# Kernel optimization log

Measured on AMD Instinct MI355X. Metric: run time of the kernel, lower is better.

The kernel has to match this reference:

```python
import jax, jax.numpy as jnp
import numpy as np

B, C, H, W = 8, 256, 128, 128
K = 3  # conv kernel size, padding=1 -> SAME


def conv3x3(x, w, b):
    # x: [B,C,H,W], w: [O,I,K,K], b: [O]
    y = jax.lax.conv_general_dilated(
        x, w, window_strides=(1, 1), padding='SAME',
        dimension_numbers=('NCHW', 'OIHW', 'NCHW'))
    return y + b[None, :, None, None]


def setup_inputs() -> dict:
    key = jax.random.key(0)
    ks = jax.random.split(key, 7)
    fan_in = C * K * K
    s = 1.0 / np.sqrt(fan_in)
    x = jax.random.normal(ks[0], (B, C, H, W), dtype=jnp.float32)
    Wq = jax.random.uniform(ks[1], (C, C, K, K), jnp.float32, -s, s)
    bq = jax.random.uniform(ks[2], (C,), jnp.float32, -s, s)
    Wk = jax.random.uniform(ks[3], (C, C, K, K), jnp.float32, -s, s)
    bk = jax.random.uniform(ks[4], (C,), jnp.float32, -s, s)
    Wv = jax.random.uniform(ks[5], (C, C, K, K), jnp.float32, -s, s)
    bv = jax.random.uniform(ks[6], (C,), jnp.float32, -s, s)
    return {'x': x, 'Wq': Wq, 'bq': bq, 'Wk': Wk, 'bk': bk, 'Wv': Wv, 'bv': bv}


def reference(x, Wq, bq, Wk, bk, Wv, bv):
    b_, c_, h_, w_ = x.shape
    residual = x
    q = jax.nn.relu(conv3x3(x, Wq, bq))  # [B,C,H,W]
    k = jax.nn.relu(conv3x3(x, Wk, bk))  # [B,C,H,W]
    v = conv3x3(x, Wv, bv)               # [B,C,H,W]
    # per-(batch,channel) spatial matmul: [H,W] @ [H,W] -> [H,W] (requires H==W)
    attn = jnp.einsum('bcij,bcjk->bcik', q, k)
    # softmax over the flattened H*W positions jointly per (b,c)
    attn = jax.nn.softmax(attn.reshape(b_, c_, h_ * w_), axis=-1).reshape(b_, c_, h_, w_)
    y = jnp.einsum('bcij,bcjk->bcik', attn, v)
    return y + residual
```

## Files before the change

kernel.cpp:

```cpp
#include <hip/hip_runtime.h>

#define BB 8
#define CC 256
#define HH 128
#define WW 128
#define HW (HH*WW)

typedef float f32x4 __attribute__((ext_vector_type(4)));
typedef float f32x16 __attribute__((ext_vector_type(16)));
typedef short s16x8 __attribute__((ext_vector_type(8)));

__device__ inline unsigned short f2bf(float f) {
  union { float f; unsigned int u; } un;
  un.f = f;
  unsigned int u = un.u;
  return (unsigned short)((u + 0x7fffu + ((u >> 16) & 1u)) >> 16);
}

__device__ __forceinline__ void gload_lds16(const void* g, void* l) {
  __builtin_amdgcn_global_load_lds(
      (const __attribute__((address_space(1))) unsigned int*)g,
      (__attribute__((address_space(3))) unsigned int*)l, 16, 0, 0);
}

__global__ __launch_bounds__(256) void k_prepass(const float* __restrict__ x,
                                                 unsigned short* __restrict__ xbf) {
  __shared__ float tile[64][68];
  int bh = blockIdx.x;
  int b = bh >> 7, h = bh & 127;
  int w0 = blockIdx.y * 64;
  int c0 = blockIdx.z * 64;
  int t = threadIdx.x;
  {
    int c = t >> 2, wq = (t & 3) << 4;
    const float4* src = reinterpret_cast<const float4*>(
        x + (((size_t)(b * CC + c0 + c) * HH + h) * WW + w0 + wq));
    float4 v0 = src[0], v1 = src[1], v2 = src[2], v3 = src[3];
    *reinterpret_cast<float4*>(&tile[c][wq + 0])  = v0;
    *reinterpret_cast<float4*>(&tile[c][wq + 4])  = v1;
    *reinterpret_cast<float4*>(&tile[c][wq + 8])  = v2;
    *reinterpret_cast<float4*>(&tile[c][wq + 12]) = v3;
  }
  __syncthreads();
  {
    int w = t >> 2, cg = (t & 3) << 4;
    unsigned short tmp[16];
#pragma unroll
    for (int i = 0; i < 16; ++i) tmp[i] = f2bf(tile[cg + i][w]);
    unsigned short* dst = xbf + ((size_t)(b * HH + h) * WW + w0 + w) * CC + c0 + cg;
    *reinterpret_cast<int4*>(dst)     = *reinterpret_cast<int4*>(tmp);
    *reinterpret_cast<int4*>(dst + 8) = *reinterpret_cast<int4*>(tmp + 8);
  }
}

__global__ __launch_bounds__(256) void k_repack(const float* __restrict__ Wq,
                                                const float* __restrict__ Wk,
                                                const float* __restrict__ Wv,
                                                unsigned short* __restrict__ Wp,
                                                unsigned short* __restrict__ zp) {
  if (blockIdx.x == 0 && threadIdx.x < 64) {
    int4 z = {0, 0, 0, 0};
    reinterpret_cast<int4*>(zp)[threadIdx.x] = z;
  }
  int idx = blockIdx.x * 256 + threadIdx.x;
  if (idx >= 8 * 9 * 768 * 32) return;
  int ci = idx & 31;
  int tmp = idx >> 5;
  int focs = tmp % 768;
  int tmp2 = tmp / 768;
  int tap = tmp2 % 9;
  int chunk = tmp2 / 9;
  int cv = focs >> 8, oc = focs & 255;
  int cin = chunk * 32 + ci;
  const float* Wsrc = (cv == 0) ? Wq : ((cv == 1) ? Wk : Wv);
  Wp[idx] = f2bf(Wsrc[(size_t)(oc * 256 + cin) * 9 + tap]);
}

__global__ __launch_bounds__(256, 2) void k_conv(const unsigned short* __restrict__ xbf,
                                                 const unsigned short* __restrict__ Wp,
                                                 const unsigned short* __restrict__ zp,
                                                 const float* __restrict__ bq,
                                                 const float* __restrict__ bk,
                                                 const float* __restrict__ bv,
                                                 unsigned short* __restrict__ qkv) {
  __shared__ unsigned short xs[2][4][132][32];
  __shared__ float bias_s[128];
  int bid = blockIdx.x;
  int v_ = (bid & 7) * 384 + (bid >> 3);
  int mtile = v_ % 6;
  int bhp = v_ / 6;
  int b = bhp >> 6;
  int h0 = (bhp & 63) * 2;
  int t = threadIdx.x;
  int lane = t & 63, wave = t >> 6;
  int wm = wave >> 1, wq = wave & 1;
  int l31 = lane & 31, lg1 = lane >> 5;

  if (t < 128) {
    int focs = mtile * 128 + t;
    int cv = focs >> 8, oc = focs & 255;
    const float* bp = (cv == 0) ? bq : ((cv == 1) ? bk : bv);
    bias_s[t] = bp[oc];
  }
  {
    int cell = t >> 4;
    int bf_ = cell >> 3, r_ = (cell >> 1) & 3;
    int wc_ = (cell & 1) ? 129 : 0;
    *reinterpret_cast<int*>(reinterpret_cast<char*>(&xs[bf_][r_][wc_][0]) + (t & 15) * 4) = 0;
  }

  int l2 = lane >> 2, l4 = lane & 3;
  int osw = l4 ^ (((l2 + 1) >> 1) & 3);
  int rsta = wave;
  int hin = h0 + rsta - 1;
  bool inb = ((unsigned)hin < 128u);
  const unsigned short* srow =
      xbf + ((size_t)(b * HH + (inb ? hin : 0)) * WW + l2) * CC + osw * 8;
  const unsigned short* zsrc = zp + lane * 8;

  auto STAGE = [&](int bufn, int chunk) {
    char* d0 = reinterpret_cast<char*>(&xs[bufn][rsta][1][0]);
    if (inb) {
      const unsigned short* s0 = srow + chunk * 32;
#pragma unroll
      for (int j = 0; j < 8; ++j)
        gload_lds16(s0 + j * (16 * CC), d0 + j * 1024);
    } else {
#pragma unroll
      for (int j = 0; j < 8; ++j)
        gload_lds16(zsrc, d0 + j * 1024);
    }
  };

  f32x16 acc[2][2][2] = {};
  STAGE(0, 0);
  __syncthreads();
  int buf = 0;
  for (int chunk = 0; chunk < 8; ++chunk) {
    if (chunk < 7) STAGE(buf ^ 1, chunk + 1);
    const unsigned short (*xsb)[132][32] = xs[buf];
    const unsigned short* ap0 = Wp + (size_t)chunk * (9 * 768 * 32)
        + (size_t)(mtile * 128 + wm * 64 + l31) * 32 + lg1 * 8;
#pragma unroll
    for (int ss = 0; ss < 3; ++ss) {
#pragma unroll
      for (int kk = 0; kk < 2; ++kk) {
        s16x8 Bf[4][2];
#pragma unroll
        for (int rin = 0; rin < 4; ++rin)
#pragma unroll
        for (int nt = 0; nt < 2; ++nt) {
          int wc = wq * 64 + nt * 32 + l31 + ss;
          int pslot = (kk * 2 + lg1) ^ ((wc >> 1) & 3);
          Bf[rin][nt] = *reinterpret_cast<const s16x8*>(
              reinterpret_cast<const char*>(&xsb[rin][0][0]) + wc * 64 + pslot * 16);
        }
        s16x8 Af[3][2];
#pragma unroll
        for (int rr = 0; rr < 3; ++rr)
#pragma unroll
        for (int mt = 0; mt < 2; ++mt)
          Af[rr][mt] = *reinterpret_cast<const s16x8*>(
              ap0 + (rr * 3 + ss) * (768 * 32) + mt * 1024 + kk * 16);
#pragma unroll
        for (int rr = 0; rr < 3; ++rr)
#pragma unroll
        for (int row = 0; row < 2; ++row)
#pragma unroll
        for (int mt = 0; mt < 2; ++mt)
#pragma unroll
        for (int nt = 0; nt < 2; ++nt)
          acc[mt][row][nt] = __builtin_amdgcn_mfma_f32_32x32x16_bf16(
              Af[rr][mt], Bf[row + rr][nt], acc[mt][row][nt], 0, 0, 0);
      }
    }
    if (chunk < 7) __syncthreads();
    buf ^= 1;
  }

#pragma unroll
  for (int mt = 0; mt < 2; ++mt) {
#pragma unroll
    for (int row = 0; row < 2; ++row) {
#pragma unroll
      for (int nt = 0; nt < 2; ++nt) {
        int wcol = wq * 64 + nt * 32 + l31;
        int h = h0 + row;
#pragma unroll
        for (int reg = 0; reg < 16; ++reg) {
          int rloc = (reg & 3) + 8 * (reg >> 2) + 4 * lg1;
          int floc = wm * 64 + mt * 32 + rloc;
          float vv = acc[mt][row][nt][reg] + bias_s[floc];
          int focs = mtile * 128 + floc;
          if (focs < 512) vv = fmaxf(vv, 0.0f);
          int cv = focs >> 8, oc = focs & 255;
          qkv[(size_t)(cv * 2048 + b * 256 + oc) * HW + h * WW + wcol] = f2bf(vv);
        }
      }
    }
  }
}

#define PADA 136
__global__ __launch_bounds__(256) void k_attn(const unsigned short* __restrict__ qkv,
                                              const float* __restrict__ x,
                                              float* __restrict__ out) {
  __shared__ unsigned short al[128][PADA];
  __shared__ unsigned short kt[128][PADA];
  __shared__ unsigned short vt[128][PADA];
  __shared__ float red[8];
  int bc = blockIdx.x;
  const unsigned short* qp = qkv + (size_t)bc * HW;
  const unsigned short* kp = qkv + (size_t)(2048 + bc) * HW;
  const unsigned short* vp = qkv + (size_t)(4096 + bc) * HW;
  int t = threadIdx.x;
  for (int g = t; g < HW; g += 256) {
    int row = g >> 7, col = g & 127;
    kt[col][row] = kp[g];
    vt[col][row] = vp[g];
  }
  __syncthreads();
  int lane = t & 63, wave = t >> 6;
  int wm = wave >> 1, wn = wave & 1;
  int l15 = lane & 15, lg = lane >> 4;
  f32x4 acc[4][4] = {};
#pragma unroll
  for (int kk = 0; kk < 4; ++kk) {
    s16x8 af[4], bfr[4];
#pragma unroll
    for (int m = 0; m < 4; ++m)
      af[m] = *reinterpret_cast<const s16x8*>(qp + (size_t)(wm * 64 + m * 16 + l15) * WW + kk * 32 + lg * 8);
#pragma unroll
    for (int n = 0; n < 4; ++n)
      bfr[n] = *reinterpret_cast<const s16x8*>(&kt[wn * 64 + n * 16 + l15][kk * 32 + lg * 8]);
#pragma unroll
    for (int m = 0; m < 4; ++m)
#pragma unroll
      for (int n = 0; n < 4; ++n)
        acc[m][n] = __builtin_amdgcn_mfma_f32_16x16x32_bf16(af[m], bfr[n], acc[m][n], 0, 0, 0);
  }
  float lm = -3.0e38f;
#pragma unroll
  for (int m = 0; m < 4; ++m)
#pragma unroll
    for (int n = 0; n < 4; ++n)
#pragma unroll
      for (int rg = 0; rg < 4; ++rg)
        lm = fmaxf(lm, acc[m][n][rg]);
  for (int off = 32; off > 0; off >>= 1) lm = fmaxf(lm, __shfl_xor(lm, off));
  if (lane == 0) red[wave] = lm;
  __syncthreads();
  float M = fmaxf(fmaxf(red[0], red[1]), fmaxf(red[2], red[3]));
  float ls = 0.0f;
#pragma unroll
  for (int m = 0; m < 4; ++m)
#pragma unroll
    for (int n = 0; n < 4; ++n)
#pragma unroll
      for (int rg = 0; rg < 4; ++rg)
        ls += __expf(acc[m][n][rg] - M);
  for (int off = 32; off > 0; off >>= 1) ls += __shfl_xor(ls, off);
  if (lane == 0) red[4 + wave] = ls;
  __syncthreads();
  float inv = 1.0f / (red[4] + red[5] + red[6] + red[7]);
#pragma unroll
  for (int m = 0; m < 4; ++m) {
#pragma unroll
    for (int n = 0; n < 4; ++n) {
      int col = wn * 64 + n * 16 + l15;
#pragma unroll
      for (int rg = 0; rg < 4; ++rg) {
        int row = wm * 64 + m * 16 + lg * 4 + rg;
        al[row][col] = f2bf(__expf(acc[m][n][rg] - M) * inv);
      }
    }
  }
  __syncthreads();
  f32x4 o_[4][4] = {};
#pragma unroll
  for (int kk = 0; kk < 4; ++kk) {
    s16x8 af[4], bfr[4];
#pragma unroll
    for (int m = 0; m < 4; ++m)
      af[m] = *reinterpret_cast<const s16x8*>(&al[wm * 64 + m * 16 + l15][kk * 32 + lg * 8]);
#pragma unroll
    for (int n = 0; n < 4; ++n)
      bfr[n] = *reinterpret_cast<const s16x8*>(&vt[wn * 64 + n * 16 + l15][kk * 32 + lg * 8]);
#pragma unroll
    for (int m = 0; m < 4; ++m)
#pragma unroll
      for (int n = 0; n < 4; ++n)
        o_[m][n] = __builtin_amdgcn_mfma_f32_16x16x32_bf16(af[m], bfr[n], o_[m][n], 0, 0, 0);
  }
  const float* xp = x + (size_t)bc * HW;
  float* op = out + (size_t)bc * HW;
#pragma unroll
  for (int m = 0; m < 4; ++m) {
#pragma unroll
    for (int n = 0; n < 4; ++n) {
      int col = wn * 64 + n * 16 + l15;
#pragma unroll
      for (int rg = 0; rg < 4; ++rg) {
        int row = wm * 64 + m * 16 + lg * 4 + rg;
        op[row * WW + col] = o_[m][n][rg] + xp[row * WW + col];
      }
    }
  }
}

extern "C" void kernel_launch(void* const* d_in, const int* in_sizes, int n_in,
                              void* d_out, int out_size, void* d_ws, size_t ws_size,
                              hipStream_t stream) {
  const float* x  = (const float*)d_in[0];
  const float* Wq = (const float*)d_in[1];
  const float* bq = (const float*)d_in[2];
  const float* Wk = (const float*)d_in[3];
  const float* bk = (const float*)d_in[4];
  const float* Wv = (const float*)d_in[5];
  const float* bv = (const float*)d_in[6];
  float* out = (float*)d_out;

  unsigned short* xbf = (unsigned short*)d_ws;
  unsigned short* qkv = xbf + (size_t)33554432;
  unsigned short* Wp  = qkv + (size_t)3 * 33554432;
  unsigned short* zp  = Wp + (size_t)(8 * 9 * 768 * 32);

  dim3 g0(1024, 2, 4);
  k_prepass<<<g0, 256, 0, stream>>>(x, xbf);
  k_repack<<<6912, 256, 0, stream>>>(Wq, Wk, Wv, Wp, zp);
  k_conv<<<3072, 256, 0, stream>>>(xbf, Wp, zp, bq, bk, bv, qkv);
  k_attn<<<2048, 256, 0, stream>>>(qkv, x, out);
}
```

Baseline: 575.5 us.

## Software-pipeline weight fragment loads and interleave LDS staging with MFMA phases

Restructures the conv GEMM main loop so the weight (A) fragments for the next k-step are loaded from global memory into a double-buffered register set while the current step's MFMAs run. The next chunk's global-to-LDS staging is split into pairs of loads spread across the first four phases. Sched barriers and s_setprio around the MFMA block control instruction ordering and wave priority. The chunk-end sync is replaced by an explicit partial vmcnt wait plus s_barrier. This aims to hide global load latency behind math, at the cost of more registers and a hand-tuned waitcnt that must match the number of outstanding loads.

Result: slower. 606.1 us (+5.3%).

```diff
diff --git a/kernel.cpp b/kernel.cpp
--- a/kernel.cpp
+++ b/kernel.cpp
@@ -111,71 +111,97 @@
 
   int l2 = lane >> 2, l4 = lane & 3;
   int osw = l4 ^ (((l2 + 1) >> 1) & 3);
-  int rsta = wave;
-  int hin = h0 + rsta - 1;
+  int hin = h0 + wave - 1;
   bool inb = ((unsigned)hin < 128u);
   const unsigned short* srow =
       xbf + ((size_t)(b * HH + (inb ? hin : 0)) * WW + l2) * CC + osw * 8;
   const unsigned short* zsrc = zp + lane * 8;
 
-  auto STAGE = [&](int bufn, int chunk) {
-    char* d0 = reinterpret_cast<char*>(&xs[bufn][rsta][1][0]);
+  const size_t CH_STRIDE = (size_t)9 * 768 * 32;
+  const unsigned short* apbase = Wp + (size_t)(mtile * 128 + wm * 64 + l31) * 32 + lg1 * 8;
+
+  f32x16 acc[2][2][2] = {};
+  s16x8 Afb[2][3][2];
+
+  {
+    char* d0 = reinterpret_cast<char*>(&xs[0][wave][1][0]);
     if (inb) {
-      const unsigned short* s0 = srow + chunk * 32;
-#pragma unroll
-      for (int j = 0; j < 8; ++j)
-        gload_lds16(s0 + j * (16 * CC), d0 + j * 1024);
+#pragma unroll
+      for (int j = 0; j < 8; ++j) gload_lds16(srow + j * (16 * CC), d0 + j * 1024);
     } else {
 #pragma unroll
-      for (int j = 0; j < 8; ++j)
-        gload_lds16(zsrc, d0 + j * 1024);
-    }
-  };
-
-  f32x16 acc[2][2][2] = {};
-  STAGE(0, 0);
-  __syncthreads();
-  int buf = 0;
+      for (int j = 0; j < 8; ++j) gload_lds16(zsrc, d0 + j * 1024);
+    }
+  }
+#pragma unroll
+  for (int rr = 0; rr < 3; ++rr)
+#pragma unroll
+  for (int mt = 0; mt < 2; ++mt)
+    Afb[0][rr][mt] = *reinterpret_cast<const s16x8*>(apbase + (rr * 3) * (768 * 32) + mt * 1024);
+  __syncthreads();
+
   for (int chunk = 0; chunk < 8; ++chunk) {
-    if (chunk < 7) STAGE(buf ^ 1, chunk + 1);
-    const unsigned short (*xsb)[132][32] = xs[buf];
-    const unsigned short* ap0 = Wp + (size_t)chunk * (9 * 768 * 32)
-        + (size_t)(mtile * 128 + wm * 64 + l31) * 32 + lg1 * 8;
-#pragma unroll
-    for (int ss = 0; ss < 3; ++ss) {
-#pragma unroll
-      for (int kk = 0; kk < 2; ++kk) {
-        s16x8 Bf[4][2];
-#pragma unroll
-        for (int rin = 0; rin < 4; ++rin)
-#pragma unroll
-        for (int nt = 0; nt < 2; ++nt) {
-          int wc = wq * 64 + nt * 32 + l31 + ss;
-          int pslot = (kk * 2 + lg1) ^ ((wc >> 1) & 3);
-          Bf[rin][nt] = *reinterpret_cast<const s16x8*>(
-              reinterpret_cast<const char*>(&xsb[rin][0][0]) + wc * 64 + pslot * 16);
+    const int buf = chunk & 1;
+    const unsigned short* ap_cur = apbase + chunk * CH_STRIDE;
+    const unsigned short* ap_nxt = (chunk < 7) ? ap_cur + CH_STRIDE : ap_cur;
+    const char* xsb = reinterpret_cast<const char*>(&xs[buf][0][0][0]);
+    char* dstg = reinterpret_cast<char*>(&xs[buf ^ 1][wave][1][0]);
+    const unsigned short* sstg = srow + (chunk + 1) * 32;
+
+#pragma unroll
+    for (int p = 0; p < 6; ++p) {
+      const int ss = p >> 1, kk = p & 1;
+      s16x8 Bf[4][2];
+#pragma unroll
+      for (int rin = 0; rin < 4; ++rin)
+#pragma unroll
+      for (int nt = 0; nt < 2; ++nt) {
+        int wc = wq * 64 + nt * 32 + l31 + ss;
+        int pslot = (kk * 2 + lg1) ^ ((wc >> 1) & 3);
+        Bf[rin][nt] = *reinterpret_cast<const s16x8*>(
+            xsb + rin * (132 * 64) + wc * 64 + pslot * 16);
+      }
+      {
+        const int pn = (p + 1) % 6, ssn = pn >> 1, kkn = pn & 1;
+        const unsigned short* apn = (p == 5) ? ap_nxt : ap_cur;
+#pragma unroll
+        for (int rr = 0; rr < 3; ++rr)
+#pragma unroll
+        for (int mt = 0; mt < 2; ++mt)
+          Afb[(p + 1) & 1][rr][mt] = *reinterpret_cast<const s16x8*>(
+              apn + (rr * 3 + ssn) * (768 * 32) + mt * 1024 + kkn * 16);
+      }
+      __builtin_amdgcn_sched_barrier(0);
+      if (p < 4 && chunk < 7) {
+        if (inb) {
+          gload_lds16(sstg + (2 * p) * (16 * CC), dstg + (2 * p) * 1024);
+          gload_lds16(sstg + (2 * p + 1) * (16 * CC), dstg + (2 * p + 1) * 1024);
+        } else {
+          gload_lds16(zsrc, dstg + (2 * p) * 1024);
+          gload_lds16(zsrc, dstg + (2 * p + 1) * 1024);
         }
-        s16x8 Af[3][2];
-#pragma unroll
-        for (int rr = 0; rr < 3; ++rr)
-#pragma unroll
-        for (int mt = 0; mt < 2; ++mt)
-          Af[rr][mt] = *reinterpret_cast<const s16x8*>(
-              ap0 + (rr * 3 + ss) * (768 * 32) + mt * 1024 + kk * 16);
-#pragma unroll
-        for (int rr = 0; rr < 3; ++rr)
-#pragma unroll
-        for (int row = 0; row < 2; ++row)
-#pragma unroll
-        for (int mt = 0; mt < 2; ++mt)
-#pragma unroll
-        for (int nt = 0; nt < 2; ++nt)
-          acc[mt][row][nt] = __builtin_amdgcn_mfma_f32_32x32x16_bf16(
-              Af[rr][mt], Bf[row + rr][nt], acc[mt][row][nt], 0, 0, 0);
-      }
-    }
-    if (chunk < 7) __syncthreads();
-    buf ^= 1;
+      }
+      __builtin_amdgcn_sched_barrier(0);
+      __builtin_amdgcn_s_setprio(1);
+#pragma unroll
+      for (int rr = 0; rr < 3; ++rr)
+#pragma unroll
+      for (int row = 0; row < 2; ++row)
+#pragma unroll
+      for (int mt = 0; mt < 2; ++mt)
+#pragma unroll
+      for (int nt = 0; nt < 2; ++nt)
+        acc[mt][row][nt] = __builtin_amdgcn_mfma_f32_32x32x16_bf16(
+            Afb[p & 1][rr][mt], Bf[row + rr][nt], acc[mt][row][nt], 0, 0, 0);
+      __builtin_amdgcn_s_setprio(0);
+      __builtin_amdgcn_sched_barrier(0);
+    }
+    if (chunk < 7) {
+      asm volatile("s_waitcnt vmcnt(12)" ::: "memory");
+      __builtin_amdgcn_s_barrier();
+      asm volatile("" ::: "memory");
+      __builtin_amdgcn_sched_barrier(0);
+    }
   }
 
 #pragma unroll
```

## Restructure conv kernel to 8 waves with per-wave LDS staging and software pipelining

Applied to the files above, without the earlier changes.

The conv kernel moves from 4 to 8 waves per block. Each wave stages its own 32-column slab plus halo of input rows into a private LDS region, so the block-wide barriers inside the channel loop go away. A and B fragments are double-buffered in registers across six unrolled sub-steps, with sched barriers, setprio and explicit waitcnt so the next chunk's global-to-LDS loads overlap the MFMAs. Each wave now covers 64 filters by 32 columns instead of 64 by 64, so it loads more overlapping halo data and more redundant weight fragments per MFMA, and register pressure rises at 512 threads.

Measured after the change: 713.4 us. +24.0%, slower.

```diff
diff --git a/kernel.cpp b/kernel.cpp
--- a/kernel.cpp
+++ b/kernel.cpp
@@ -76,14 +76,14 @@
   Wp[idx] = f2bf(Wsrc[(size_t)(oc * 256 + cin) * 9 + tap]);
 }
 
-__global__ __launch_bounds__(256, 2) void k_conv(const unsigned short* __restrict__ xbf,
+__global__ __launch_bounds__(512, 2) void k_conv(const unsigned short* __restrict__ xbf,
                                                  const unsigned short* __restrict__ Wp,
                                                  const unsigned short* __restrict__ zp,
                                                  const float* __restrict__ bq,
                                                  const float* __restrict__ bk,
                                                  const float* __restrict__ bv,
                                                  unsigned short* __restrict__ qkv) {
-  __shared__ unsigned short xs[2][4][132][32];
+  __shared__ unsigned short xs[8][4][48][32];
   __shared__ float bias_s[128];
   int bid = blockIdx.x;
   int v_ = (bid & 7) * 384 + (bid >> 3);
@@ -93,7 +93,7 @@
   int h0 = (bhp & 63) * 2;
   int t = threadIdx.x;
   int lane = t & 63, wave = t >> 6;
-  int wm = wave >> 1, wq = wave & 1;
+  int s = wave & 3, fh = wave >> 2;
   int l31 = lane & 31, lg1 = lane >> 5;
 
   if (t < 128) {
@@ -102,100 +102,108 @@
     const float* bp = (cv == 0) ? bq : ((cv == 1) ? bk : bv);
     bias_s[t] = bp[oc];
   }
-  {
-    int cell = t >> 4;
-    int bf_ = cell >> 3, r_ = (cell >> 1) & 3;
-    int wc_ = (cell & 1) ? 129 : 0;
-    *reinterpret_cast<int*>(reinterpret_cast<char*>(&xs[bf_][r_][wc_][0]) + (t & 15) * 4) = 0;
-  }
-
-  int l2 = lane >> 2, l4 = lane & 3;
-  int osw = l4 ^ (((l2 + 1) >> 1) & 3);
-  int rsta = wave;
-  int hin = h0 + rsta - 1;
-  bool inb = ((unsigned)hin < 128u);
-  const unsigned short* srow =
-      xbf + ((size_t)(b * HH + (inb ? hin : 0)) * WW + l2) * CC + osw * 8;
+  __syncthreads();
+
+  int oct = (lane & 3) ^ ((lane >> 3) & 3);
+  int lane_off = ((lane >> 2) << 8) + (oct << 3);
+  int wbase = s * 32 - 8;
   const unsigned short* zsrc = zp + lane * 8;
-
-  auto STAGE = [&](int bufn, int chunk) {
-    char* d0 = reinterpret_cast<char*>(&xs[bufn][rsta][1][0]);
-    if (inb) {
-      const unsigned short* s0 = srow + chunk * 32;
-#pragma unroll
-      for (int j = 0; j < 8; ++j)
-        gload_lds16(s0 + j * (16 * CC), d0 + j * 1024);
-    } else {
-#pragma unroll
-      for (int j = 0; j < 8; ++j)
-        gload_lds16(zsrc, d0 + j * 1024);
+  char* myxs = (char*)&xs[wave][0][0][0];
+
+  const size_t CH_STRIDE = (size_t)9 * 768 * 32;
+  const unsigned short* apbase = Wp + (size_t)(mtile * 128 + fh * 64 + l31) * 32 + lg1 * 8;
+
+  auto STAGE = [&](int c) {
+#pragma unroll
+    for (int r = 0; r < 4; ++r) {
+      int hin = h0 + r - 1;
+      bool rv = ((unsigned)hin < 128u);
+      const unsigned short* rowp =
+          xbf + (size_t)(b * HH + (rv ? hin : 0)) * WW * CC + c * 32;
+#pragma unroll
+      for (int j = 0; j < 3; ++j) {
+        int wl = wbase + j * 16 + (lane >> 2);
+        bool v = rv && ((unsigned)wl < 128u);
+        const unsigned short* p =
+            v ? (rowp + (ptrdiff_t)(wbase + j * 16) * CC + lane_off) : zsrc;
+        gload_lds16(p, myxs + r * 3072 + j * 1024);
+      }
     }
   };
-
-  f32x16 acc[2][2][2] = {};
-  STAGE(0, 0);
-  __syncthreads();
-  int buf = 0;
+  auto BREAD = [&](s16x8 (&Bf)[4], int un) {
+    const int ss = un >> 1, kk = un & 1;
+    const int col = l31 + ss + 7;
+    const int slot = (kk * 2 + lg1) ^ ((col >> 1) & 3);
+#pragma unroll
+    for (int rin = 0; rin < 4; ++rin)
+      Bf[rin] = *reinterpret_cast<const s16x8*>(myxs + rin * 3072 + col * 64 + slot * 16);
+  };
+  auto ALOAD = [&](s16x8 (&Af)[3][2], const unsigned short* ap, int un) {
+    const int ss = un >> 1, kk = un & 1;
+#pragma unroll
+    for (int rr = 0; rr < 3; ++rr)
+#pragma unroll
+      for (int mt = 0; mt < 2; ++mt)
+        Af[rr][mt] = *reinterpret_cast<const s16x8*>(
+            ap + (rr * 3 + ss) * (768 * 32) + mt * 1024 + kk * 16);
+  };
+
+  f32x16 acc[2][2] = {};
+  s16x8 Bfb[2][4];
+  s16x8 Afb[2][3][2];
+
+  STAGE(0);
+  ALOAD(Afb[0], apbase, 0);
+  asm volatile("s_waitcnt vmcnt(6)" ::: "memory");
+  BREAD(Bfb[0], 0);
+
   for (int chunk = 0; chunk < 8; ++chunk) {
-    if (chunk < 7) STAGE(buf ^ 1, chunk + 1);
-    const unsigned short (*xsb)[132][32] = xs[buf];
-    const unsigned short* ap0 = Wp + (size_t)chunk * (9 * 768 * 32)
-        + (size_t)(mtile * 128 + wm * 64 + l31) * 32 + lg1 * 8;
-#pragma unroll
-    for (int ss = 0; ss < 3; ++ss) {
-#pragma unroll
-      for (int kk = 0; kk < 2; ++kk) {
-        s16x8 Bf[4][2];
-#pragma unroll
-        for (int rin = 0; rin < 4; ++rin)
-#pragma unroll
-        for (int nt = 0; nt < 2; ++nt) {
-          int wc = wq * 64 + nt * 32 + l31 + ss;
-          int pslot = (kk * 2 + lg1) ^ ((wc >> 1) & 3);
-          Bf[rin][nt] = *reinterpret_cast<const s16x8*>(
-              reinterpret_cast<const char*>(&xsb[rin][0][0]) + wc * 64 + pslot * 16);
-        }
-        s16x8 Af[3][2];
-#pragma unroll
-        for (int rr = 0; rr < 3; ++rr)
-#pragma unroll
-        for (int mt = 0; mt < 2; ++mt)
-          Af[rr][mt] = *reinterpret_cast<const s16x8*>(
-              ap0 + (rr * 3 + ss) * (768 * 32) + mt * 1024 + kk * 16);
-#pragma unroll
-        for (int rr = 0; rr < 3; ++rr)
+    const unsigned short* ap_cur = apbase + chunk * CH_STRIDE;
+#pragma unroll
+    for (int u = 0; u < 6; ++u) {
+      if (u < 5) {
+        ALOAD(Afb[(u + 1) & 1], ap_cur, u + 1);
+        BREAD(Bfb[(u + 1) & 1], u + 1);
+      } else if (chunk < 7) {
+        asm volatile("s_waitcnt lgkmcnt(0)" ::: "memory");
+        __builtin_amdgcn_sched_barrier(0);
+        STAGE(chunk + 1);
+        ALOAD(Afb[0], ap_cur + CH_STRIDE, 0);
+      }
+      __builtin_amdgcn_sched_barrier(0);
+      __builtin_amdgcn_s_setprio(1);
+#pragma unroll
+      for (int rr = 0; rr < 3; ++rr)
 #pragma unroll
         for (int row = 0; row < 2; ++row)
 #pragma unroll
-        for (int mt = 0; mt < 2; ++mt)
-#pragma unroll
-        for (int nt = 0; nt < 2; ++nt)
-          acc[mt][row][nt] = __builtin_amdgcn_mfma_f32_32x32x16_bf16(
-              Af[rr][mt], Bf[row + rr][nt], acc[mt][row][nt], 0, 0, 0);
-      }
-    }
-    if (chunk < 7) __syncthreads();
-    buf ^= 1;
-  }
-
+          for (int mt = 0; mt < 2; ++mt)
+            acc[mt][row] = __builtin_amdgcn_mfma_f32_32x32x16_bf16(
+                Afb[u & 1][rr][mt], Bfb[u & 1][row + rr], acc[mt][row], 0, 0, 0);
+      __builtin_amdgcn_s_setprio(0);
+      __builtin_amdgcn_sched_barrier(0);
+    }
+    if (chunk < 7) {
+      asm volatile("s_waitcnt vmcnt(6)" ::: "memory");
+      BREAD(Bfb[0], 0);
+    }
+  }
+
+  int wcol = s * 32 + l31;
 #pragma unroll
   for (int mt = 0; mt < 2; ++mt) {
 #pragma unroll
     for (int row = 0; row < 2; ++row) {
-#pragma unroll
-      for (int nt = 0; nt < 2; ++nt) {
-        int wcol = wq * 64 + nt * 32 + l31;
-        int h = h0 + row;
-#pragma unroll
-        for (int reg = 0; reg < 16; ++reg) {
-          int rloc = (reg & 3) + 8 * (reg >> 2) + 4 * lg1;
-          int floc = wm * 64 + mt * 32 + rloc;
-          float vv = acc[mt][row][nt][reg] + bias_s[floc];
-          int focs = mtile * 128 + floc;
-          if (focs < 512) vv = fmaxf(vv, 0.0f);
-          int cv = focs >> 8, oc = focs & 255;
-          qkv[(size_t)(cv * 2048 + b * 256 + oc) * HW + h * WW + wcol] = f2bf(vv);
-        }
+      int h = h0 + row;
+#pragma unroll
+      for (int reg = 0; reg < 16; ++reg) {
+        int rloc = (reg & 3) + 8 * (reg >> 2) + 4 * lg1;
+        int floc = fh * 64 + mt * 32 + rloc;
+        float vv = acc[mt][row][reg] + bias_s[floc];
+        int focs = mtile * 128 + floc;
+        if (focs < 512) vv = fmaxf(vv, 0.0f);
+        int cv = focs >> 8, oc = focs & 255;
+        qkv[(size_t)(cv * 2048 + b * 256 + oc) * HW + h * WW + wcol] = f2bf(vv);
       }
     }
   }
@@ -328,6 +336,6 @@
   dim3 g0(1024, 2, 4);
   k_prepass<<<g0, 256, 0, stream>>>(x, xbf);
   k_repack<<<6912, 256, 0, stream>>>(Wq, Wk, Wv, Wp, zp);
-  k_conv<<<3072, 256, 0, stream>>>(xbf, Wp, zp, bq, bk, bv, qkv);
+  k_conv<<<3072, 512, 0, stream>>>(xbf, Wp, zp, bq, bk, bv, qkv);
   k_attn<<<2048, 256, 0, stream>>>(qkv, x, out);
 }
```
